# Optimization experiments

Hardware: AMD Instinct MI355X
Metric: run time of the kernel (lower is better)

Reference implementation:

```python
import jax, jax.numpy as jnp
import numpy as np

N, M, D, E = 16384, 8192, 8, 2_000_000
DELTA = 1.0   # init arg delta
P = 1.0       # init arg p (forced to 1 in __init__)
EPS = 1e-6


def setup_inputs() -> dict:
    key = jax.random.key(0)
    ks = jax.random.split(key, 7)
    return {
        "gamma_rows": jax.random.normal(ks[0], (N,), dtype=jnp.float32),
        "gamma_cols": jax.random.normal(ks[1], (M,), dtype=jnp.float32),
        "latent_z": jax.random.uniform(ks[2], (N, D), dtype=jnp.float32),
        "latent_w": jax.random.uniform(ks[3], (M, D), dtype=jnp.float32),
        "weights": jax.random.uniform(ks[4], (E,), dtype=jnp.float32),
        "rows_idx": jax.random.randint(ks[5], (E,), 0, N, dtype=jnp.int32),
        "col_idx": jax.random.randint(ks[6], (E,), 0, M, dtype=jnp.int32),
    }


def reference(gamma_rows, gamma_cols, latent_z, latent_w, weights, rows_idx, col_idx):
    # Simplex projections (Softmax over latent dim)
    z = jax.nn.softmax(latent_z, axis=1)   # [N, D]
    w = jax.nn.softmax(latent_w, axis=1)   # [M, D]

    # torch.cdist(z, w, p=2): full N x M euclidean distance matrix
    sq = (jnp.sum(z * z, axis=1)[:, None]
          + jnp.sum(w * w, axis=1)[None, :]
          - 2.0 * (z @ w.T))                       # [N, M]
    dist = jnp.sqrt(jnp.maximum(sq, 0.0))          # [N, M]
    dist_matrix = -DELTA * (dist + EPS)            # [N, M]

    # z_pdist1 = exp(gamma_rows) @ exp(dist_matrix) @ exp(gamma_cols)
    z_pdist1 = jnp.einsum("i,ij,j->", jnp.exp(gamma_rows),
                          jnp.exp(dist_matrix), jnp.exp(gamma_cols))

    # Edge (link) term: per-edge euclidean distance between gathered embeddings
    delta_latent = jnp.sqrt(jnp.sum((z[rows_idx] - w[col_idx]) ** 2, axis=-1))  # [E]
    z_pdist2 = jnp.sum(weights * (gamma_rows[rows_idx] + gamma_cols[col_idx]
                                  - (DELTA * delta_latent) ** P))

    return -z_pdist2 + z_pdist1
```

## Files before the change

### kernel.cpp

```cpp
#include <hip/hip_runtime.h>
#include <math.h>

#define N_ROWS 16384
#define M_COLS 8192
#define TPB 256
#define IT 4
#define JT 64
#define NJ (M_COLS / JT)
#define NIB (N_ROWS / (TPB * IT))
#define PAIR_BLOCKS (NIB * NJ)
#define EDGE_BLOCKS 2048
#define EU 4
#define GRID_BLOCKS (PAIR_BLOCKS + EDGE_BLOCKS)

typedef float v2f __attribute__((ext_vector_type(2)));
typedef _Float16 h8 __attribute__((ext_vector_type(8)));

#define C2 2.0813689810056077f

__global__ __launch_bounds__(TPB) void rownorm_kernel(
    const float* __restrict__ lz, const float* __restrict__ gr,
    const float* __restrict__ lw, const float* __restrict__ gc,
    float* __restrict__ z, float* __restrict__ zz, float* __restrict__ eg,
    _Float16* __restrict__ zh,
    float* __restrict__ w, float* __restrict__ ww, float* __restrict__ ec,
    _Float16* __restrict__ wh)
{
    int gi = blockIdx.x * TPB + threadIdx.x;
    const float *src, *g;
    float *dv, *dq, *de;
    _Float16* dh;
    int i;
    if (gi < N_ROWS) { src = lz; g = gr; dv = z; dq = zz; de = eg; dh = zh; i = gi; }
    else             { src = lw; g = gc; dv = w; dq = ww; de = ec; dh = wh; i = gi - N_ROWS; }

    const float4* sp = (const float4*)(src + (size_t)i * 8);
    float4 a = sp[0], b = sp[1];
    float v[8] = {a.x, a.y, a.z, a.w, b.x, b.y, b.z, b.w};
    float m = v[0];
    #pragma unroll
    for (int d = 1; d < 8; d++) m = fmaxf(m, v[d]);
    float s = 0.f;
    #pragma unroll
    for (int d = 0; d < 8; d++) { v[d] = __expf(v[d] - m); s += v[d]; }
    float inv = 1.f / s;
    float sq = 0.f;
    h8 hv;
    #pragma unroll
    for (int d = 0; d < 8; d++) {
        v[d] *= inv;
        sq = fmaf(v[d], v[d], sq);
        hv[d] = (_Float16)v[d];
    }
    float4 o0 = {v[0], v[1], v[2], v[3]};
    float4 o1 = {v[4], v[5], v[6], v[7]};
    float4* dp = (float4*)(dv + (size_t)i * 8);
    dp[0] = o0; dp[1] = o1;
    *(h8*)(dh + (size_t)i * 8) = hv;
    dq[i] = C2 * sq;
    de[i] = __expf(g[i]);
}

__global__ __launch_bounds__(TPB) void fused_kernel(
    const float* __restrict__ z, const float* __restrict__ zz,
    const float* __restrict__ eg,
    const float* __restrict__ w, const float* __restrict__ ww,
    const float* __restrict__ ec,
    const _Float16* __restrict__ zh, const _Float16* __restrict__ wh,
    const float* __restrict__ gr, const float* __restrict__ gc,
    const float* __restrict__ wt,
    const int* __restrict__ ridx, const int* __restrict__ cidx, int E,
    double* __restrict__ pair_part, double* __restrict__ edge_part)
{
    __shared__ float  sw[JT * 8];
    __shared__ float  swq[JT];
    __shared__ float  sec[JT];
    __shared__ double sred[TPB];

    const int t   = threadIdx.x;
    const int bid = blockIdx.x;
    const int rid = bid >> 1;

    if ((bid & 1) == 0) {
        const int ib = rid / NJ;
        const int jb = rid - ib * NJ;
        const int j0 = jb * JT;

        if (t < JT * 2) ((float4*)sw)[t] = ((const float4*)(w + (size_t)j0 * 8))[t];
        if (t < JT)     { swq[t] = ww[j0 + t]; sec[t] = ec[j0 + t]; }

        v2f  zi[IT][4];
        float zzi[IT], acc[IT];
        const int ibase = ib * (TPB * IT);
        #pragma unroll
        for (int k = 0; k < IT; k++) {
            int i = ibase + k * TPB + t;
            const float4* zp = (const float4*)(z + (size_t)i * 8);
            float4 a = zp[0], b = zp[1];
            zi[k][0] = (v2f){-2.f * C2 * a.x, -2.f * C2 * a.y};
            zi[k][1] = (v2f){-2.f * C2 * a.z, -2.f * C2 * a.w};
            zi[k][2] = (v2f){-2.f * C2 * b.x, -2.f * C2 * b.y};
            zi[k][3] = (v2f){-2.f * C2 * b.z, -2.f * C2 * b.w};
            zzi[k] = zz[i];
            acc[k] = 0.f;
        }
        __syncthreads();

        const float4* s4 = (const float4*)sw;
        for (int j = 0; j < JT; j++) {
            float4 wa = s4[j * 2];
            float4 wb = s4[j * 2 + 1];
            v2f w01 = {wa.x, wa.y}, w23 = {wa.z, wa.w};
            v2f w45 = {wb.x, wb.y}, w67 = {wb.z, wb.w};
            float wq = swq[j];
            float e  = sec[j];
            #pragma unroll
            for (int k = 0; k < IT; k++) {
                v2f p = {zzi[k], wq};
                p = __builtin_elementwise_fma(zi[k][0], w01, p);
                p = __builtin_elementwise_fma(zi[k][1], w23, p);
                p = __builtin_elementwise_fma(zi[k][2], w45, p);
                p = __builtin_elementwise_fma(zi[k][3], w67, p);
                float sq = fmaxf(p.x + p.y, 0.f);
                float d, pr;
                asm("v_sqrt_f32 %0, %1" : "=v"(d) : "v"(sq));
                asm("v_exp_f32 %0, -%1" : "=v"(pr) : "v"(d));
                acc[k] = fmaf(e, pr, acc[k]);
            }
        }

        double tp = 0.0;
        #pragma unroll
        for (int k = 0; k < IT; k++) {
            int i = ibase + k * TPB + t;
            tp += (double)eg[i] * (double)acc[k];
        }

        sred[t] = tp;
        __syncthreads();
        for (int s = TPB / 2; s > 0; s >>= 1) {
            if (t < s) sred[t] += sred[t + s];
            __syncthreads();
        }
        if (t == 0) pair_part[rid] = sred[0];
    } else {
        const int tid = rid * TPB + t;
        const int e0 = tid * EU;
        double local = 0.0;
        if (e0 < E) {
            int4   rr  = *(const int4*)(ridx + e0);
            int4   cc  = *(const int4*)(cidx + e0);
            float4 wt4 = *(const float4*)(wt + e0);
            int   r[EU]  = {rr.x, rr.y, rr.z, rr.w};
            int   c[EU]  = {cc.x, cc.y, cc.z, cc.w};
            float wv[EU] = {wt4.x, wt4.y, wt4.z, wt4.w};
            h8 zr[EU], wr[EU];
            float grv[EU], gcv[EU];
            #pragma unroll
            for (int u = 0; u < EU; u++) {
                zr[u]  = *(const h8*)(zh + (size_t)r[u] * 8);
                wr[u]  = *(const h8*)(wh + (size_t)c[u] * 8);
                grv[u] = gr[r[u]];
                gcv[u] = gc[c[u]];
            }
            #pragma unroll
            for (int u = 0; u < EU; u++) {
                h8 dv = zr[u] - wr[u];
                float s = 0.f;
                #pragma unroll
                for (int qd = 0; qd < 8; qd++) {
                    float f = (float)dv[qd];
                    s = fmaf(f, f, s);
                }
                float dist;
                asm("v_sqrt_f32 %0, %1" : "=v"(dist) : "v"(s));
                local += (double)(wv[u] * (grv[u] + gcv[u] - dist));
            }
        }
        sred[t] = local;
        __syncthreads();
        for (int s2 = TPB / 2; s2 > 0; s2 >>= 1) {
            if (t < s2) sred[t] += sred[t + s2];
            __syncthreads();
        }
        if (t == 0) edge_part[rid] = sred[0];
    }
}

__global__ __launch_bounds__(TPB) void final_kernel(
    const double* __restrict__ pp, int np,
    const double* __restrict__ ep, int ne,
    float* __restrict__ out)
{
    __shared__ double sred[TPB];
    const int t = threadIdx.x;
    double s1 = 0.0, s2 = 0.0;
    for (int i = t; i < np; i += TPB) s1 += pp[i];
    for (int i = t; i < ne; i += TPB) s2 += ep[i];
    sred[t] = s1;
    __syncthreads();
    for (int s = TPB / 2; s > 0; s >>= 1) {
        if (t < s) sred[t] += sred[t + s];
        __syncthreads();
    }
    double pair_sum = sred[0];
    __syncthreads();
    sred[t] = s2;
    __syncthreads();
    for (int s = TPB / 2; s > 0; s >>= 1) {
        if (t < s) sred[t] += sred[t + s];
        __syncthreads();
    }
    if (t == 0) {
        double edge_sum = sred[0];
        double cf = exp(-1.0e-6);
        out[0] = (float)(cf * pair_sum - edge_sum);
    }
}

extern "C" void kernel_launch(void* const* d_in, const int* in_sizes, int n_in,
                              void* d_out, int out_size, void* d_ws, size_t ws_size,
                              hipStream_t stream)
{
    const float* gamma_rows = (const float*)d_in[0];
    const float* gamma_cols = (const float*)d_in[1];
    const float* latent_z   = (const float*)d_in[2];
    const float* latent_w   = (const float*)d_in[3];
    const float* weights    = (const float*)d_in[4];
    const int*   rows_idx   = (const int*)d_in[5];
    const int*   col_idx    = (const int*)d_in[6];
    float* out = (float*)d_out;
    const int E = in_sizes[4];

    char* base = (char*)d_ws;
    size_t off = 0;
    float* z  = (float*)(base + off); off += (size_t)N_ROWS * 8 * 4;
    float* zz = (float*)(base + off); off += (size_t)N_ROWS * 4;
    float* eg = (float*)(base + off); off += (size_t)N_ROWS * 4;
    float* w  = (float*)(base + off); off += (size_t)M_COLS * 8 * 4;
    float* ww = (float*)(base + off); off += (size_t)M_COLS * 4;
    float* ec = (float*)(base + off); off += (size_t)M_COLS * 4;
    _Float16* zh = (_Float16*)(base + off); off += (size_t)N_ROWS * 8 * 2;
    _Float16* wh = (_Float16*)(base + off); off += (size_t)M_COLS * 8 * 2;
    double* pair_part = (double*)(base + off); off += (size_t)PAIR_BLOCKS * 8;
    double* edge_part = (double*)(base + off); off += (size_t)EDGE_BLOCKS * 8;
    (void)ws_size;

    rownorm_kernel<<<(N_ROWS + M_COLS) / TPB, TPB, 0, stream>>>(
        latent_z, gamma_rows, latent_w, gamma_cols,
        z, zz, eg, zh, w, ww, ec, wh);
    fused_kernel<<<GRID_BLOCKS, TPB, 0, stream>>>(
        z, zz, eg, w, ww, ec, zh, wh, gamma_rows, gamma_cols,
        weights, rows_idx, col_idx, E, pair_part, edge_part);
    final_kernel<<<1, TPB, 0, stream>>>(pair_part, PAIR_BLOCKS,
                                        edge_part, EDGE_BLOCKS, out);
}
```

Measured before the change: 175.3 us.

## Fuse softmax row normalization into main kernel and drop precompute pass

Removes the separate row-normalization kernel and recomputes the softmax, squared norms and exp(gamma) inside the pair and edge blocks of a single kernel. The pair blocks normalize their z rows and w tiles on the fly. The edge blocks now gather fp32 raw latents and apply softmax per edge instead of reading precomputed fp16 embeddings. This saves one launch and the intermediate global writes, but each edge gathers twice the bytes and does redundant exp work, and w tiles are renormalized in every pair block.

```diff
diff --git a/kernel.cpp b/kernel.cpp
--- a/kernel.cpp
+++ b/kernel.cpp
@@ -14,29 +14,10 @@
 #define GRID_BLOCKS (PAIR_BLOCKS + EDGE_BLOCKS)
 
 typedef float v2f __attribute__((ext_vector_type(2)));
-typedef _Float16 h8 __attribute__((ext_vector_type(8)));
 
 #define C2 2.0813689810056077f
 
-__global__ __launch_bounds__(TPB) void rownorm_kernel(
-    const float* __restrict__ lz, const float* __restrict__ gr,
-    const float* __restrict__ lw, const float* __restrict__ gc,
-    float* __restrict__ z, float* __restrict__ zz, float* __restrict__ eg,
-    _Float16* __restrict__ zh,
-    float* __restrict__ w, float* __restrict__ ww, float* __restrict__ ec,
-    _Float16* __restrict__ wh)
-{
-    int gi = blockIdx.x * TPB + threadIdx.x;
-    const float *src, *g;
-    float *dv, *dq, *de;
-    _Float16* dh;
-    int i;
-    if (gi < N_ROWS) { src = lz; g = gr; dv = z; dq = zz; de = eg; dh = zh; i = gi; }
-    else             { src = lw; g = gc; dv = w; dq = ww; de = ec; dh = wh; i = gi - N_ROWS; }
-
-    const float4* sp = (const float4*)(src + (size_t)i * 8);
-    float4 a = sp[0], b = sp[1];
-    float v[8] = {a.x, a.y, a.z, a.w, b.x, b.y, b.z, b.w};
+__device__ inline void softmax8(float v[8]) {
     float m = v[0];
     #pragma unroll
     for (int d = 1; d < 8; d++) m = fmaxf(m, v[d]);
@@ -44,30 +25,13 @@
     #pragma unroll
     for (int d = 0; d < 8; d++) { v[d] = __expf(v[d] - m); s += v[d]; }
     float inv = 1.f / s;
-    float sq = 0.f;
-    h8 hv;
     #pragma unroll
-    for (int d = 0; d < 8; d++) {
-        v[d] *= inv;
-        sq = fmaf(v[d], v[d], sq);
-        hv[d] = (_Float16)v[d];
-    }
-    float4 o0 = {v[0], v[1], v[2], v[3]};
-    float4 o1 = {v[4], v[5], v[6], v[7]};
-    float4* dp = (float4*)(dv + (size_t)i * 8);
-    dp[0] = o0; dp[1] = o1;
-    *(h8*)(dh + (size_t)i * 8) = hv;
-    dq[i] = C2 * sq;
-    de[i] = __expf(g[i]);
-}
-
-__global__ __launch_bounds__(TPB) void fused_kernel(
-    const float* __restrict__ z, const float* __restrict__ zz,
-    const float* __restrict__ eg,
-    const float* __restrict__ w, const float* __restrict__ ww,
-    const float* __restrict__ ec,
-    const _Float16* __restrict__ zh, const _Float16* __restrict__ wh,
-    const float* __restrict__ gr, const float* __restrict__ gc,
+    for (int d = 0; d < 8; d++) v[d] *= inv;
+}
+
+__global__ __launch_bounds__(TPB) void mega_kernel(
+    const float* __restrict__ lz, const float* __restrict__ gr,
+    const float* __restrict__ lw, const float* __restrict__ gc,
     const float* __restrict__ wt,
     const int* __restrict__ ridx, const int* __restrict__ cidx, int E,
     double* __restrict__ pair_part, double* __restrict__ edge_part)
@@ -86,8 +50,20 @@
         const int jb = rid - ib * NJ;
         const int j0 = jb * JT;
 
-        if (t < JT * 2) ((float4*)sw)[t] = ((const float4*)(w + (size_t)j0 * 8))[t];
-        if (t < JT)     { swq[t] = ww[j0 + t]; sec[t] = ec[j0 + t]; }
+        if (t < JT) {
+            const float4* wp = (const float4*)(lw + (size_t)(j0 + t) * 8);
+            float4 a = wp[0], b = wp[1];
+            float v[8] = {a.x, a.y, a.z, a.w, b.x, b.y, b.z, b.w};
+            softmax8(v);
+            float sq = 0.f;
+            #pragma unroll
+            for (int d = 0; d < 8; d++) {
+                sw[t * 8 + d] = v[d];
+                sq = fmaf(v[d], v[d], sq);
+            }
+            swq[t] = C2 * sq;
+            sec[t] = __expf(gc[j0 + t]);
+        }
 
         v2f  zi[IT][4];
         float zzi[IT], acc[IT];
@@ -95,13 +71,18 @@
         #pragma unroll
         for (int k = 0; k < IT; k++) {
             int i = ibase + k * TPB + t;
-            const float4* zp = (const float4*)(z + (size_t)i * 8);
+            const float4* zp = (const float4*)(lz + (size_t)i * 8);
             float4 a = zp[0], b = zp[1];
-            zi[k][0] = (v2f){-2.f * C2 * a.x, -2.f * C2 * a.y};
-            zi[k][1] = (v2f){-2.f * C2 * a.z, -2.f * C2 * a.w};
-            zi[k][2] = (v2f){-2.f * C2 * b.x, -2.f * C2 * b.y};
-            zi[k][3] = (v2f){-2.f * C2 * b.z, -2.f * C2 * b.w};
-            zzi[k] = zz[i];
+            float v[8] = {a.x, a.y, a.z, a.w, b.x, b.y, b.z, b.w};
+            softmax8(v);
+            float sq = 0.f;
+            #pragma unroll
+            for (int d = 0; d < 8; d++) sq = fmaf(v[d], v[d], sq);
+            zi[k][0] = (v2f){-2.f * C2 * v[0], -2.f * C2 * v[1]};
+            zi[k][1] = (v2f){-2.f * C2 * v[2], -2.f * C2 * v[3]};
+            zi[k][2] = (v2f){-2.f * C2 * v[4], -2.f * C2 * v[5]};
+            zi[k][3] = (v2f){-2.f * C2 * v[6], -2.f * C2 * v[7]};
+            zzi[k] = C2 * sq;
             acc[k] = 0.f;
         }
         __syncthreads();
@@ -133,7 +114,7 @@
         #pragma unroll
         for (int k = 0; k < IT; k++) {
             int i = ibase + k * TPB + t;
-            tp += (double)eg[i] * (double)acc[k];
+            tp += (double)__expf(gr[i]) * (double)acc[k];
         }
 
         sred[t] = tp;
@@ -154,27 +135,39 @@
             int   r[EU]  = {rr.x, rr.y, rr.z, rr.w};
             int   c[EU]  = {cc.x, cc.y, cc.z, cc.w};
             float wv[EU] = {wt4.x, wt4.y, wt4.z, wt4.w};
-            h8 zr[EU], wr[EU];
-            float grv[EU], gcv[EU];
-            #pragma unroll
-            for (int u = 0; u < EU; u++) {
-                zr[u]  = *(const h8*)(zh + (size_t)r[u] * 8);
-                wr[u]  = *(const h8*)(wh + (size_t)c[u] * 8);
-                grv[u] = gr[r[u]];
-                gcv[u] = gc[c[u]];
-            }
-            #pragma unroll
-            for (int u = 0; u < EU; u++) {
-                h8 dv = zr[u] - wr[u];
-                float s = 0.f;
+            #pragma unroll
+            for (int half = 0; half < 2; half++) {
+                float4 za[2], zb[2], wa4[2], wb4[2];
+                float grv[2], gcv[2];
                 #pragma unroll
-                for (int qd = 0; qd < 8; qd++) {
-                    float f = (float)dv[qd];
-                    s = fmaf(f, f, s);
+                for (int u2 = 0; u2 < 2; u2++) {
+                    int u = half * 2 + u2;
+                    const float4* zp = (const float4*)(lz + (size_t)r[u] * 8);
+                    const float4* wp = (const float4*)(lw + (size_t)c[u] * 8);
+                    za[u2] = zp[0]; zb[u2] = zp[1];
+                    wa4[u2] = wp[0]; wb4[u2] = wp[1];
+                    grv[u2] = gr[r[u]];
+                    gcv[u2] = gc[c[u]];
                 }
-                float dist;
-                asm("v_sqrt_f32 %0, %1" : "=v"(dist) : "v"(s));
-                local += (double)(wv[u] * (grv[u] + gcv[u] - dist));
+                #pragma unroll
+                for (int u2 = 0; u2 < 2; u2++) {
+                    int u = half * 2 + u2;
+                    float vz[8] = {za[u2].x, za[u2].y, za[u2].z, za[u2].w,
+                                   zb[u2].x, zb[u2].y, zb[u2].z, zb[u2].w};
+                    float vw[8] = {wa4[u2].x, wa4[u2].y, wa4[u2].z, wa4[u2].w,
+                                   wb4[u2].x, wb4[u2].y, wb4[u2].z, wb4[u2].w};
+                    softmax8(vz);
+                    softmax8(vw);
+                    float s = 0.f;
+                    #pragma unroll
+                    for (int qd = 0; qd < 8; qd++) {
+                        float f = vz[qd] - vw[qd];
+                        s = fmaf(f, f, s);
+                    }
+                    float dist;
+                    asm("v_sqrt_f32 %0, %1" : "=v"(dist) : "v"(s));
+                    local += (double)(wv[u] * (grv[u2] + gcv[u2] - dist));
+                }
             }
         }
         sred[t] = local;
@@ -233,24 +226,12 @@
     const int E = in_sizes[4];
 
     char* base = (char*)d_ws;
-    size_t off = 0;
-    float* z  = (float*)(base + off); off += (size_t)N_ROWS * 8 * 4;
-    float* zz = (float*)(base + off); off += (size_t)N_ROWS * 4;
-    float* eg = (float*)(base + off); off += (size_t)N_ROWS * 4;
-    float* w  = (float*)(base + off); off += (size_t)M_COLS * 8 * 4;
-    float* ww = (float*)(base + off); off += (size_t)M_COLS * 4;
-    float* ec = (float*)(base + off); off += (size_t)M_COLS * 4;
-    _Float16* zh = (_Float16*)(base + off); off += (size_t)N_ROWS * 8 * 2;
-    _Float16* wh = (_Float16*)(base + off); off += (size_t)M_COLS * 8 * 2;
-    double* pair_part = (double*)(base + off); off += (size_t)PAIR_BLOCKS * 8;
-    double* edge_part = (double*)(base + off); off += (size_t)EDGE_BLOCKS * 8;
+    double* pair_part = (double*)base;
+    double* edge_part = (double*)(base + (size_t)PAIR_BLOCKS * 8);
     (void)ws_size;
 
-    rownorm_kernel<<<(N_ROWS + M_COLS) / TPB, TPB, 0, stream>>>(
+    mega_kernel<<<GRID_BLOCKS, TPB, 0, stream>>>(
         latent_z, gamma_rows, latent_w, gamma_cols,
-        z, zz, eg, zh, w, ww, ec, wh);
-    fused_kernel<<<GRID_BLOCKS, TPB, 0, stream>>>(
-        z, zz, eg, w, ww, ec, zh, wh, gamma_rows, gamma_cols,
         weights, rows_idx, col_idx, E, pair_part, edge_part);
     final_kernel<<<1, TPB, 0, stream>>>(pair_part, PAIR_BLOCKS,
                                         edge_part, EDGE_BLOCKS, out);
```

After: 179.3 us. +2.3%, slower.
